# Performance work log

Hardware: AMD Instinct MI355X
Metric: run time of the kernel (lower is better)

## Reference

```python
import jax, jax.numpy as jnp
import numpy as np

B, T, H, W, P = 2, 4, 224, 224, 16
D, DI, NS, RK, KC = 768, 1536, 16, 48, 4
DEPTH = 16
NV, NA = 196, 24                 # video/audio patches per frame
NTOT = (NV + 2 + NA + 2) * T     # 896 tokens (cls + patches + global, both modalities)
LVIS = NTOT // 2                 # 448 visible tokens


def setup_inputs():
    key = jax.random.key(0)
    ks = iter(jax.random.split(key, 64))
    def nrm(shape, s=0.02):
        return jax.random.normal(next(ks), shape, jnp.float32) * s
    inp = {}
    inp['x_v'] = jax.random.normal(next(ks), (B, 3, T, H, W), jnp.float32)
    inp['x_a'] = jax.random.normal(next(ks), (B, 64, 96 * T), jnp.float32)
    inp['patch_v_w'] = nrm((D, 3, P, P)); inp['patch_v_b'] = jnp.zeros((D,), jnp.float32)
    inp['patch_a_w'] = nrm((D, 1, P, P)); inp['patch_a_b'] = jnp.zeros((D,), jnp.float32)
    inp['pos_v'] = nrm((1, NV, D)); inp['pos_a'] = nrm((1, NA, D))
    inp['tpos_v'] = nrm((1, T, D)); inp['tpos_a'] = nrm((1, T, D))
    inp['cls_v'] = nrm((1, 1, D)); inp['cls_a'] = nrm((1, 1, D))
    inp['glob_v'] = nrm((1, 1, D)); inp['glob_a'] = nrm((1, 1, D))
    inp['norm_w'] = jnp.ones((DEPTH, D), jnp.float32)
    inp['in_w'] = nrm((DEPTH, 2 * DI, D))
    inp['conv_w'] = nrm((DEPTH, DI, KC), 0.2); inp['conv_b'] = jnp.zeros((DEPTH, DI), jnp.float32)
    inp['conv_w_b'] = nrm((DEPTH, DI, KC), 0.2); inp['conv_b_b'] = jnp.zeros((DEPTH, DI), jnp.float32)
    inp['xproj_w'] = nrm((DEPTH, RK + 2 * NS, DI))
    inp['xproj_w_b'] = nrm((DEPTH, RK + 2 * NS, DI))
    inp['dt_w'] = nrm((DEPTH, DI, RK), 0.1)
    inp['dt_w_b'] = nrm((DEPTH, DI, RK), 0.1)
    # mamba dt-bias init: inverse-softplus of dt ~ logU[1e-3, 0.1]
    lo, hi = np.log(1e-3), np.log(0.1)
    u = jax.random.uniform(next(ks), (DEPTH, DI), jnp.float32)
    dt = jnp.exp(u * (hi - lo) + lo)
    inp['dt_b'] = dt + jnp.log(-jnp.expm1(-dt))
    u2 = jax.random.uniform(next(ks), (DEPTH, DI), jnp.float32)
    dt2 = jnp.exp(u2 * (hi - lo) + lo)
    inp['dt_b_b'] = dt2 + jnp.log(-jnp.expm1(-dt2))
    alog = jnp.log(jnp.arange(1, NS + 1, dtype=jnp.float32))  # S4D-real init
    inp['A_log'] = jnp.broadcast_to(alog, (DEPTH, DI, NS)) + 0.0
    inp['A_log_b'] = jnp.broadcast_to(alog, (DEPTH, DI, NS)) + 0.0
    inp['D_par'] = jnp.ones((DEPTH, DI), jnp.float32)
    inp['D_par_b'] = jnp.ones((DEPTH, DI), jnp.float32)
    inp['out_w'] = nrm((DEPTH, D, DI))
    rng = np.random.default_rng(0)
    vi = np.stack([np.sort(rng.choice(NTOT, LVIS, replace=False)) for _ in range(B)])
    inp['vis_idx'] = jnp.asarray(vi, jnp.int32)
    return inp


def _causal_conv1d(x, w, b):
    # x: [B,L,DI]; depthwise causal conv, kernel KC
    xt = x.transpose(0, 2, 1)
    y = jax.lax.conv_general_dilated(xt, w[:, None, :], (1,), [(KC - 1, 0)], feature_group_count=DI)
    return (y + b[None, :, None]).transpose(0, 2, 1)


def _ssd(xc, dt, Bm, Cm, A, Dp):
    # selective scan: xc,dt [B,L,DI]; Bm,Cm [B,L,NS]; A [DI,NS]
    dA = jnp.exp(dt[..., None] * A)                         # B,L,DI,NS
    dBx = dt[..., None] * Bm[:, :, None, :] * xc[..., None]
    def step(h, s):
        a, bx, c = s
        h = a * h + bx
        return h, jnp.einsum('bdn,bn->bd', h, c)
    h0 = jnp.zeros((xc.shape[0], DI, NS), xc.dtype)
    _, ys = jax.lax.scan(step, h0, (jnp.swapaxes(dA, 0, 1), jnp.swapaxes(dBx, 0, 1), jnp.swapaxes(Cm, 0, 1)))
    return jnp.swapaxes(ys, 0, 1) + xc * Dp


def _mamba_dir(xi, zi, cw, cb, xw, dw, db, alog, dp):
    xc = jax.nn.silu(_causal_conv1d(xi, cw, cb))
    proj = jnp.einsum('bld,ed->ble', xc, xw)
    dtr, Bm, Cm = jnp.split(proj, [RK, RK + NS], axis=-1)
    dt = jax.nn.softplus(jnp.einsum('blr,dr->bld', dtr, dw) + db)
    y = _ssd(xc, dt, Bm, Cm, -jnp.exp(alog), dp)
    return y * jax.nn.silu(zi)


def reference(x_v, x_a, patch_v_w, patch_v_b, patch_a_w, patch_a_b, pos_v, pos_a, tpos_v, tpos_a,
              cls_v, cls_a, glob_v, glob_a, norm_w, in_w, conv_w, conv_b, conv_w_b, conv_b_b,
              xproj_w, xproj_w_b, dt_w, dt_b, dt_w_b, dt_b_b, A_log, A_log_b, D_par, D_par_b,
              out_w, vis_idx):
    Bn = x_v.shape[0]
    # video patch embed: conv3d k=(1,16,16) as unfold + matmul
    xv = x_v.transpose(0, 2, 3, 4, 1).reshape(Bn, T, H // P, P, W // P, P, 3)
    xv = xv.transpose(0, 1, 2, 4, 3, 5, 6).reshape(Bn, T, NV, P * P * 3)
    wv = patch_v_w.transpose(0, 2, 3, 1).reshape(D, -1)   # (kh,kw,c) flattening order
    xv = xv @ wv.T + patch_v_b                            # B,T,196,D
    # audio patch embed: [B,64,TA] -> [B,1,TA,64] conv2d 16x16
    TA = x_a.shape[-1]
    xa = x_a.transpose(0, 2, 1).reshape(Bn, TA // P, P, 64 // P, P)
    xa = xa.transpose(0, 1, 3, 2, 4).reshape(Bn, (TA // P) * (64 // P), P * P)
    xa = xa @ patch_a_w.reshape(D, -1).T + patch_a_b      # B, T*24, D
    xa = xa.reshape(Bn, T, NA, D)
    # spatial + temporal positional embeddings
    xv = xv + pos_v[None] + tpos_v[:, :, None, :]
    xa = xa + pos_a[None] + tpos_a[:, :, None, :]
    def add_tokens(x, cls, glob):
        BT = x.shape[0]
        return jnp.concatenate([jnp.broadcast_to(cls, (BT, 1, D)), x, jnp.broadcast_to(glob, (BT, 1, D))], 1)
    xv = add_tokens(xv.reshape(Bn * T, NV, D), cls_v, glob_v).reshape(Bn, T, NV + 2, D)
    xa = add_tokens(xa.reshape(Bn * T, NA, D), cls_a, glob_a).reshape(Bn, T, NA + 2, D)
    x = jnp.concatenate([xv, xa], 2).reshape(Bn, -1, D)   # B, 896, D
    x_vis = jnp.take_along_axis(x, vis_idx[:, :, None], axis=1)  # B, 448, D (x[~mask])

    def layer(carry, p):
        h, res = carry
        nw, iw, cw, cb, cwb, cbb, xw, xwb, dw, db, dwb, dbb, al, alb, dp, dpb, ow = p
        res = h + res                                     # fused add (drop_path=identity at eval)
        hn = res * jax.lax.rsqrt(jnp.mean(res * res, -1, keepdims=True) + 1e-5) * nw  # RMSNorm
        xz = jnp.einsum('bld,ed->ble', hn, iw)
        xi, zi = jnp.split(xz, 2, axis=-1)
        yf = _mamba_dir(xi, zi, cw, cb, xw, dw, db, al, dp)
        yb = _mamba_dir(xi[:, ::-1], zi[:, ::-1], cwb, cbb, xwb, dwb, dbb, alb, dpb)
        h = jnp.einsum('bld,ed->ble', yf + yb[:, ::-1], ow)
        return (h, res), None

    carry = (x_vis, jnp.zeros_like(x_vis))
    (h, res), _ = jax.lax.scan(layer, carry, (norm_w, in_w, conv_w, conv_b, conv_w_b, conv_b_b,
                                              xproj_w, xproj_w_b, dt_w, dt_b, dt_w_b, dt_b_b,
                                              A_log, A_log_b, D_par, D_par_b, out_w))
    # clip_return_layer=1 -> return_index=[depth-1]; only the post-loop append of the
    # final residual fires, so forward_features returns stack([residual]) of shape [1,B,L,D]
    return res[None]
```

## Files before the change

### kernel.cpp

```cpp
#include <hip/hip_runtime.h>
#include <math.h>

typedef unsigned short ushort_t;
typedef __attribute__((ext_vector_type(8))) short bf16x8;
typedef __attribute__((ext_vector_type(4))) float f32x4;
typedef __attribute__((ext_vector_type(4))) unsigned short us4;

#define NBATCH 2
#define TT 4
#define DD 768
#define DI_ 1536
#define NS_ 16
#define RK_ 48
#define KC_ 4
#define DEPTH_ 16
#define NRUN 15
#define LV 448
#define NROWS (NBATCH*LV)
#define NCH 7
#define CLEN 64
#define WLAYER 4128768
#define WL4 (WLAYER/4)

__device__ __forceinline__ float silu_f(float x) { return x / (1.f + __expf(-x)); }
__device__ __forceinline__ ushort_t f2bf(float x) {
  unsigned int u = __float_as_uint(x);
  return (ushort_t)((u + 0x7FFFu + ((u >> 16) & 1u)) >> 16);
}
__device__ __forceinline__ float bf2f(ushort_t h) {
  return __uint_as_float(((unsigned int)h) << 16);
}

typedef const __attribute__((address_space(1))) unsigned int* gas1_t;
typedef __attribute__((address_space(3))) unsigned int* las3_t;
__device__ __forceinline__ void gll16(const ushort_t* g, ushort_t* l) {
  __builtin_amdgcn_global_load_lds((gas1_t)g, (las3_t)l, 16, 0, 0);
}

__global__ __launch_bounds__(256) void mfma_gemm(
    const ushort_t* __restrict__ A, const ushort_t* __restrict__ A2, int lda,
    const ushort_t* __restrict__ W, const ushort_t* __restrict__ W2, int ldw,
    const float* __restrict__ bias, const float* __restrict__ bias2,
    float* __restrict__ C, float* __restrict__ C2, int ldc,
    int M, int K, int nkChunks, long partStride, int epi)
{
  int z = blockIdx.z;
  int dir = z / nkChunks, chunk = z - dir * nkChunks;
  if (dir) { A = A2; W = W2; C = C2; bias = bias2; }
  int kChunk = K / nkChunks;
  int kbeg = chunk * kChunk;
  if (nkChunks > 1) C += (long)chunk * partStride;

  __shared__ __align__(16) ushort_t At[128 * 32];
  __shared__ __align__(16) ushort_t Bt[128 * 32];

  int tid = threadIdx.x, wv = tid >> 6, lane = tid & 63;
  int m0 = blockIdx.y * 128, n0 = blockIdx.x * 128;

  int S0 = wv * 128 + lane, S1 = S0 + 64;
  int r0 = S0 >> 2, g0 = (S0 & 3) ^ ((r0 >> 1) & 3);
  int r1 = S1 >> 2, g1 = (S1 & 3) ^ ((r1 >> 1) & 3);
  const ushort_t* a0 = A + (size_t)min(m0 + r0, M - 1) * lda + g0 * 8 + kbeg;
  const ushort_t* a1 = A + (size_t)min(m0 + r1, M - 1) * lda + g1 * 8 + kbeg;
  const ushort_t* b0 = W + (size_t)(n0 + r0) * ldw + g0 * 8 + kbeg;
  const ushort_t* b1 = W + (size_t)(n0 + r1) * ldw + g1 * 8 + kbeg;
  ushort_t* lA0 = At + S0 * 8; ushort_t* lA1 = At + S1 * 8;
  ushort_t* lB0 = Bt + S0 * 8; ushort_t* lB1 = Bt + S1 * 8;

  int wr = wv >> 1, wc = wv & 1;
  int rl = lane & 15, gl = lane >> 4;
  int offA[4], offB[4];
#pragma unroll
  for (int i = 0; i < 4; ++i) {
    int ra = wr * 64 + i * 16 + rl;
    offA[i] = ra * 32 + ((gl ^ ((ra >> 1) & 3)) * 8);
    int rb = wc * 64 + i * 16 + rl;
    offB[i] = rb * 32 + ((gl ^ ((rb >> 1) & 3)) * 8);
  }

  f32x4 acc[4][4] = {};
  int nk = kChunk >> 5;
  for (int t = 0; t < nk; ++t) {
    int ko = t << 5;
    gll16(a0 + ko, lA0); gll16(a1 + ko, lA1);
    gll16(b0 + ko, lB0); gll16(b1 + ko, lB1);
    __syncthreads();
    bf16x8 af[4], bw[4];
#pragma unroll
    for (int i = 0; i < 4; ++i) {
      af[i] = *(const bf16x8*)(At + offA[i]);
      bw[i] = *(const bf16x8*)(Bt + offB[i]);
    }
#pragma unroll
    for (int i = 0; i < 4; ++i)
#pragma unroll
      for (int j = 0; j < 4; ++j)
        acc[i][j] = __builtin_amdgcn_mfma_f32_16x16x32_bf16(af[i], bw[j], acc[i][j], 0, 0, 0);
    __syncthreads();
  }

#pragma unroll
  for (int i = 0; i < 4; ++i) {
    int row0 = m0 + wr * 64 + i * 16 + gl * 4;
#pragma unroll
    for (int q = 0; q < 4; ++q) {
      int row = row0 + q;
      if (row >= M) continue;
#pragma unroll
      for (int j = 0; j < 4; ++j) {
        int col = n0 + wc * 64 + j * 16 + rl;
        float v = acc[i][j][q];
        if (bias) v += bias[col];
        if (epi == 1) v = (v > 20.f) ? v : log1pf(__expf(v));
        if (epi == 2) ((ushort_t*)C)[(size_t)row * ldc + col] = f2bf(v);
        else C[(size_t)row * ldc + col] = v;
      }
    }
  }
}

__global__ __launch_bounds__(256) void gemm_nt(
    const float* __restrict__ A, int lda,
    const float* __restrict__ W, int ldw,
    const float* __restrict__ bias,
    float* __restrict__ C, int ldc, int M, int N, int K)
{
  __shared__ float As[16][68];
  __shared__ float Ws[16][68];
  int tid = threadIdx.x;
  int m0 = blockIdx.y * 64, n0 = blockIdx.x * 64;
  int ty = tid >> 4, tx = tid & 15;
  float acc[4][4] = {};
  for (int k0 = 0; k0 < K; k0 += 16) {
#pragma unroll
    for (int i = 0; i < 4; ++i) {
      int idx = tid + i * 256;
      int mm = idx >> 4, kk = idx & 15;
      int gm = m0 + mm, gk = k0 + kk;
      As[kk][mm] = (gm < M && gk < K) ? A[(size_t)gm * lda + gk] : 0.f;
      int gn = n0 + mm;
      Ws[kk][mm] = (gn < N && gk < K) ? W[(size_t)gn * ldw + gk] : 0.f;
    }
    __syncthreads();
#pragma unroll
    for (int kk = 0; kk < 16; ++kk) {
      float a[4], b[4];
#pragma unroll
      for (int i = 0; i < 4; ++i) a[i] = As[kk][ty * 4 + i];
#pragma unroll
      for (int j = 0; j < 4; ++j) b[j] = Ws[kk][tx * 4 + j];
#pragma unroll
      for (int i = 0; i < 4; ++i)
#pragma unroll
        for (int j = 0; j < 4; ++j) acc[i][j] = fmaf(a[i], b[j], acc[i][j]);
    }
    __syncthreads();
  }
#pragma unroll
  for (int i = 0; i < 4; ++i) {
    int gm = m0 + ty * 4 + i;
    if (gm >= M) continue;
#pragma unroll
    for (int j = 0; j < 4; ++j) {
      int gn = n0 + tx * 4 + j;
      if (gn >= N) continue;
      float v = acc[i][j];
      if (bias) v += bias[gn];
      C[(size_t)gm * ldc + gn] = v;
    }
  }
}

__global__ __launch_bounds__(256) void cast4_k(const float* __restrict__ s, ushort_t* __restrict__ d, int n4)
{
  int i = blockIdx.x * 256 + threadIdx.x;
  if (i >= n4) return;
  f32x4 v = *(const f32x4*)(s + i * 4);
  us4 o = { f2bf(v[0]), f2bf(v[1]), f2bf(v[2]), f2bf(v[3]) };
  *(us4*)(d + i * 4) = o;
}

__global__ __launch_bounds__(256) void cast_all4_k(
    const float* __restrict__ iw0, const float* __restrict__ ow0,
    const float* __restrict__ xw0, const float* __restrict__ xwb0,
    const float* __restrict__ dw0, const float* __restrict__ dwb0,
    ushort_t* __restrict__ wall, int nl)
{
  int i = blockIdx.x * 256 + threadIdx.x;
  if (i >= nl * WL4) return;
  int l = i / WL4;
  int j = (i - l * WL4) * 4;
  const float* iw  = iw0  + (size_t)l * 2359296;
  const float* ow  = ow0  + (size_t)l * 1179648;
  const float* xw  = xw0  + (size_t)l * 122880;
  const float* xwb = xwb0 + (size_t)l * 122880;
  const float* dw  = dw0  + (size_t)l * 73728;
  const float* dwb = dwb0 + (size_t)l * 73728;
  ushort_t* wb = wall + (size_t)l * WLAYER + j;
  f32x4 v = {0.f, 0.f, 0.f, 0.f};
  int j2 = j;
  if (j2 < 2359296) v = *(const f32x4*)(iw + j2);
  else {
    j2 -= 2359296;
    if (j2 < 1179648) v = *(const f32x4*)(ow + j2);
    else {
      j2 -= 1179648;
      if (j2 < 196608) { int r = j2 / 1536, k = j2 - r * 1536;
        if (r < 80) v = *(const f32x4*)(xw + r * 1536 + k); }
      else {
        j2 -= 196608;
        if (j2 < 196608) { int r = j2 / 1536, k = j2 - r * 1536;
          if (r < 80) v = *(const f32x4*)(xwb + r * 1536 + k); }
        else {
          j2 -= 196608;
          if (j2 < 98304) { int d = j2 >> 6, k = j2 & 63;
            if (k < 48) v = *(const f32x4*)(dw + d * 48 + k); }
          else { j2 -= 98304; int d = j2 >> 6, k = j2 & 63;
            if (k < 48) v = *(const f32x4*)(dwb + d * 48 + k); }
        }
      }
    }
  }
  us4 o = { f2bf(v[0]), f2bf(v[1]), f2bf(v[2]), f2bf(v[3]) };
  *(us4*)wb = o;
}

__global__ __launch_bounds__(256) void im2col_v(const float* __restrict__ xv, ushort_t* __restrict__ Av)
{
  int i = blockIdx.x * 256 + threadIdx.x;
  if (i >= 1568 * 768) return;
  int m = i / 768, k = i % 768;
  int c = k >> 8, r = k & 255;
  int kh = r >> 4, kw = r & 15;
  int bt = m / 196, n = m % 196;
  int b = bt / TT, t = bt % TT;
  int hb = n / 14, wb = n % 14;
  Av[i] = f2bf(xv[(size_t)b * 602112 + (size_t)c * 200704 + t * 50176 + (hb * 16 + kh) * 224 + wb * 16 + kw]);
}

__global__ __launch_bounds__(256) void im2col_a(const float* __restrict__ xa, float* __restrict__ Aa)
{
  int i = blockIdx.x * 256 + threadIdx.x;
  if (i >= 192 * 256) return;
  int m = i / 256, k = i % 256;
  int kh = k >> 4, kw = k & 15;
  int b = m / 96, q = m % 96;
  int tb = q >> 2, fb = q & 3;
  Aa[i] = xa[(size_t)b * 24576 + (fb * 16 + kw) * 384 + tb * 16 + kh];
}

__global__ __launch_bounds__(256) void assemble_k(
    const float* __restrict__ tokv, const float* __restrict__ toka,
    const float* __restrict__ pos_v, const float* __restrict__ pos_a,
    const float* __restrict__ tpos_v, const float* __restrict__ tpos_a,
    const float* __restrict__ cls_v, const float* __restrict__ cls_a,
    const float* __restrict__ glob_v, const float* __restrict__ glob_a,
    const int* __restrict__ vis_idx,
    float* __restrict__ h, float* __restrict__ res)
{
  int i = blockIdx.x * 256 + threadIdx.x;
  if (i >= NROWS * DD) return;
  int d = i % DD;
  int bl = i / DD;
  int r = bl % LV, b = bl / LV;
  int tok = vis_idx[b * LV + r];
  int t = tok / 224, q = tok % 224;
  float v;
  if (q == 0) v = cls_v[d];
  else if (q <= 196) {
    int n = q - 1;
    v = tokv[((size_t)(b * TT + t) * 196 + n) * DD + d] + pos_v[n * DD + d] + tpos_v[t * DD + d];
  } else if (q == 197) v = glob_v[d];
  else if (q == 198) v = cls_a[d];
  else if (q <= 222) {
    int n = q - 199;
    v = toka[((size_t)b * 96 + t * 24 + n) * DD + d] + pos_a[n * DD + d] + tpos_a[t * DD + d];
  } else v = glob_a[d];
  h[i] = v;
  res[i] = 0.f;
}

__global__ __launch_bounds__(256) void rmsnorm_k(
    const float* __restrict__ hsrc, const float* __restrict__ part,
    float* __restrict__ res, ushort_t* __restrict__ hn, const float* __restrict__ nw)
{
  int row = blockIdx.x;
  float* rp = res + (size_t)row * DD;
  ushort_t* op = hn + (size_t)row * DD;
  int tid = threadIdx.x;
  float v[3];
  float ss = 0.f;
#pragma unroll
  for (int i = 0; i < 3; ++i) {
    int c = tid + i * 256;
    float x;
    if (part) {
      x = part[(size_t)row * DD + c] + part[688128 + (size_t)row * DD + c]
        + part[2 * 688128 + (size_t)row * DD + c] + part[3 * 688128 + (size_t)row * DD + c];
    } else {
      x = hsrc[(size_t)row * DD + c];
    }
    x += rp[c];
    v[i] = x;
    ss += x * x;
  }
  for (int m = 1; m < 64; m <<= 1) ss += __shfl_xor(ss, m, 64);
  __shared__ float sred[4];
  if ((tid & 63) == 0) sred[tid >> 6] = ss;
  __syncthreads();
  float tot = sred[0] + sred[1] + sred[2] + sred[3];
  float sc = rsqrtf(tot / (float)DD + 1e-5f);
#pragma unroll
  for (int i = 0; i < 3; ++i) {
    int c = tid + i * 256;
    rp[c] = v[i];
    op[c] = f2bf(v[i] * sc * nw[c]);
  }
}

__global__ __launch_bounds__(256) void conv_k(
    const ushort_t* __restrict__ xz,
    const float* __restrict__ cw, const float* __restrict__ cb,
    const float* __restrict__ cwb, const float* __restrict__ cbb,
    ushort_t* __restrict__ xcFb, ushort_t* __restrict__ xcBb)
{
  int i = blockIdx.x * 256 + threadIdx.x;
  if (i >= NROWS * DI_) return;
  int d = i % DI_;
  int bl = i / DI_;
  int l = bl % LV, b = bl / LV;
  const ushort_t* xzb = xz + (size_t)b * LV * (2 * DI_);
  float accf = cb[d];
#pragma unroll
  for (int j = 0; j < 4; ++j) {
    int lp = l - 3 + j;
    if (lp >= 0) accf += bf2f(xzb[(size_t)lp * (2 * DI_) + d]) * cw[d * 4 + j];
  }
  float accb = cbb[d];
#pragma unroll
  for (int j = 0; j < 4; ++j) {
    int lp = l - 3 + j;
    if (lp >= 0) accb += bf2f(xzb[(size_t)(LV - 1 - lp) * (2 * DI_) + d]) * cwb[d * 4 + j];
  }
  xcFb[i] = f2bf(silu_f(accf));
  xcBb[i] = f2bf(silu_f(accb));
}

__global__ __launch_bounds__(256) void reduce_pack_k(
    const float* __restrict__ pF, const float* __restrict__ pB,
    float* __restrict__ prF, float* __restrict__ prB,
    ushort_t* __restrict__ dF, ushort_t* __restrict__ dB)
{
  int i = blockIdx.x * 256 + threadIdx.x;
  if (i >= NROWS * 128) return;
  int dir = blockIdx.y;
  const float* part = dir ? pB : pF;
  float* proj = dir ? prB : prF;
  ushort_t* dtr = dir ? dB : dF;
  int row = i >> 7, col = i & 127;
  float s = 0.f;
  if (col < 80) {
#pragma unroll
    for (int c = 0; c < 8; ++c) s += part[c * (NROWS * 128) + i];
    proj[row * 80 + col] = s;
  }
  if (col < 64) dtr[(row << 6) + col] = f2bf(col < 48 ? s : 0.f);
}

__global__ __launch_bounds__(256) void scanA_k(
    const ushort_t* __restrict__ xcFb, const float* __restrict__ dtF, const float* __restrict__ prF,
    const ushort_t* __restrict__ xcBb, const float* __restrict__ dtB, const float* __restrict__ prB,
    const float* __restrict__ AlF, const float* __restrict__ AlB,
    float* __restrict__ hloc, float* __restrict__ Pb)
{
  int dir = blockIdx.z;
  const ushort_t* xc = dir ? xcBb : xcFb;
  const float* dt = dir ? dtB : dtF;
  const float* pr = dir ? prB : prF;
  const float* Al = dir ? AlB : AlF;
  int c = blockIdx.y;
  int g = blockIdx.x * 16 + (threadIdx.x >> 4);
  int n = threadIdx.x & 15;
  int b = g / DI_, d = g % DI_;
  float An = -__expf(Al[d * NS_ + n]);
  const ushort_t* xcp = xc + (size_t)b * LV * DI_ + d;
  const float* dtp = dt + (size_t)b * LV * DI_ + d;
  const float* prp = pr + (size_t)b * LV * 80;
  int l0 = c * CLEN;
  float hs = 0.f, S = 0.f;
  float dtv = dtp[(size_t)l0 * DI_];
  float xcv = bf2f(xcp[(size_t)l0 * DI_]);
  float bn  = prp[l0 * 80 + 48 + n];
  for (int kk = 0; kk < CLEN; ++kk) {
    float dtv_n = 0.f, xcv_n = 0.f, bn_n = 0.f;
    if (kk < CLEN - 1) {
      int l1 = l0 + kk + 1;
      dtv_n = dtp[(size_t)l1 * DI_];
      xcv_n = bf2f(xcp[(size_t)l1 * DI_]);
      bn_n  = prp[l1 * 80 + 48 + n];
    }
    hs = __expf(dtv * An) * hs + dtv * bn * xcv;
    S += dtv;
    dtv = dtv_n; xcv = xcv_n; bn = bn_n;
  }
  int idx = ((dir * 3072 + g) * 6 + c) * NS_ + n;
  hloc[idx] = hs;
  Pb[idx] = __expf(An * S);
}

__global__ __launch_bounds__(256) void scanBC_k(
    const ushort_t* __restrict__ xcFb, const float* __restrict__ dtF, const float* __restrict__ prF,
    const ushort_t* __restrict__ xcBb, const float* __restrict__ dtB, const float* __restrict__ prB,
    const float* __restrict__ AlF, const float* __restrict__ AlB,
    const float* __restrict__ DpF, const float* __restrict__ DpB,
    const float* __restrict__ hloc, const float* __restrict__ Pb,
    const ushort_t* __restrict__ xz, ushort_t* __restrict__ yc)
{
  int c = blockIdx.y;
  int tid = threadIdx.x;
  int n = tid & 15, gi = (tid >> 4) & 7, dir = tid >> 7;
  int g = blockIdx.x * 8 + gi;
  int b = g / DI_, d = g % DI_;
  __shared__ float sbuf[2][8][64];

  const ushort_t* xc = dir ? xcBb : xcFb;
  const float* dt = dir ? dtB : dtF;
  const float* pr = dir ? prB : prF;
  const float* Al = dir ? AlB : AlF;
  const float* Dpp = dir ? DpB : DpF;
  int myc = dir ? (6 - c) : c;
  float An = -__expf(Al[d * NS_ + n]);
  float Dpd = Dpp[d];
  float hs = 0.f;
  for (int j = 0; j < myc; ++j) {
    int idx = ((dir * 3072 + g) * 6 + j) * NS_ + n;
    hs = Pb[idx] * hs + hloc[idx];
  }
  const ushort_t* xcp = xc + (size_t)b * LV * DI_ + d;
  const float* dtp = dt + (size_t)b * LV * DI_ + d;
  const float* prp = pr + (size_t)b * LV * 80;
  int l0 = myc * CLEN;
  float dtv = dtp[(size_t)l0 * DI_];
  float xcv = bf2f(xcp[(size_t)l0 * DI_]);
  float bn  = prp[l0 * 80 + 48 + n];
  float cn  = prp[l0 * 80 + 64 + n];
  for (int kk = 0; kk < CLEN; ++kk) {
    float dtv_n = 0.f, xcv_n = 0.f, bn_n = 0.f, cn_n = 0.f;
    if (kk < CLEN - 1) {
      int l1 = l0 + kk + 1;
      dtv_n = dtp[(size_t)l1 * DI_];
      xcv_n = bf2f(xcp[(size_t)l1 * DI_]);
      bn_n  = prp[l1 * 80 + 48 + n];
      cn_n  = prp[l1 * 80 + 64 + n];
    }
    hs = __expf(dtv * An) * hs + dtv * bn * xcv;
    float p = hs * cn;
    p += __shfl_xor(p, 1, 16);
    p += __shfl_xor(p, 2, 16);
    p += __shfl_xor(p, 4, 16);
    p += __shfl_xor(p, 8, 16);
    if (n == 0) {
      int off = dir ? (CLEN - 1 - kk) : kk;
      sbuf[dir][gi][off] = p + xcv * Dpd;
    }
    dtv = dtv_n; xcv = xcv_n; bn = bn_n; cn = cn_n;
  }
  __syncthreads();
  for (int oid = tid; oid < 512; oid += 256) {
    int gi2 = oid >> 6, kk = oid & 63;
    int g2 = blockIdx.x * 8 + gi2;
    int b2 = g2 / DI_, d2 = g2 % DI_;
    int l = c * CLEN + kk;
    float z = bf2f(xz[((size_t)b2 * LV + l) * 3072 + 1536 + d2]);
    float v = (sbuf[0][gi2][kk] + sbuf[1][gi2][kk]) * silu_f(z);
    yc[((size_t)b2 * LV + l) * DI_ + d2] = f2bf(v);
  }
}

__global__ __launch_bounds__(256) void final_k(
    const float* __restrict__ res, const float* __restrict__ part, float* __restrict__ out)
{
  int i = blockIdx.x * 256 + threadIdx.x;
  if (i >= NROWS * DD) return;
  out[i] = res[i] + part[i] + part[688128 + i] + part[2 * 688128 + i] + part[3 * 688128 + i];
}

extern "C" void kernel_launch(void* const* d_in, const int* in_sizes, int n_in,
                              void* d_out, int out_size, void* d_ws, size_t ws_size,
                              hipStream_t stream)
{
  const float* x_v = (const float*)d_in[0];
  const float* x_a = (const float*)d_in[1];
  const float* patch_v_w = (const float*)d_in[2];
  const float* patch_v_b = (const float*)d_in[3];
  const float* patch_a_w = (const float*)d_in[4];
  const float* patch_a_b = (const float*)d_in[5];
  const float* pos_v = (const float*)d_in[6];
  const float* pos_a = (const float*)d_in[7];
  const float* tpos_v = (const float*)d_in[8];
  const float* tpos_a = (const float*)d_in[9];
  const float* cls_v = (const float*)d_in[10];
  const float* cls_a = (const float*)d_in[11];
  const float* glob_v = (const float*)d_in[12];
  const float* glob_a = (const float*)d_in[13];
  const float* norm_w = (const float*)d_in[14];
  const float* in_w = (const float*)d_in[15];
  const float* conv_w = (const float*)d_in[16];
  const float* conv_b = (const float*)d_in[17];
  const float* conv_w_b = (const float*)d_in[18];
  const float* conv_b_b = (const float*)d_in[19];
  const float* xproj_w = (const float*)d_in[20];
  const float* xproj_w_b = (const float*)d_in[21];
  const float *dt_w, *dt_bias, *dt_w_b, *dt_bias_b;
  if (in_sizes[23] == DEPTH_ * DI_ * RK_) {
    dt_w = (const float*)d_in[22]; dt_w_b = (const float*)d_in[23];
    dt_bias = (const float*)d_in[24]; dt_bias_b = (const float*)d_in[25];
  } else {
    dt_w = (const float*)d_in[22]; dt_bias = (const float*)d_in[23];
    dt_w_b = (const float*)d_in[24]; dt_bias_b = (const float*)d_in[25];
  }
  const float* A_log = (const float*)d_in[26];
  const float* A_log_b = (const float*)d_in[27];
  const float* D_par = (const float*)d_in[28];
  const float* D_par_b = (const float*)d_in[29];
  const float* out_w = (const float*)d_in[30];
  const int* vis_idx = (const int*)d_in[31];

  float* ws = (float*)d_ws;
  float* res   = ws;
  float* hbuf  = ws + 688128;
  float* R1    = ws + 1376256;
  float* R2f   = ws + 4128768;
  float* R3    = ws + 4816896;
  float* xz    = ws + 7569408;
  float* dtF   = ws + 10321920;
  float* dtB   = ws + 11698176;
  float* projF = ws + 13074432;
  float* projB = ws + 13146112;
  float* wPvf  = ws + 13217792;
  float* WALLf = ws + 13512704;

  float* partF = R1;
  float* partB = R1 + 917504;
  float* hloc  = R1;
  float* Pb    = R1 + 589824;
  float* partO = R1;
  float* tokv  = R1;
  float* toka  = R1 + 1204224;
  float* Aa    = R1 + 1351680;
  ushort_t* Av_bf = (ushort_t*)xz;
  ushort_t* wPv   = (ushort_t*)wPvf;
  ushort_t* hn_bf = (ushort_t*)R2f;
  ushort_t* dtrF  = (ushort_t*)R2f;
  ushort_t* dtrB  = ((ushort_t*)R2f) + 57344;
  ushort_t* ycb   = (ushort_t*)R2f;
  ushort_t* xcFb = (ushort_t*)R3;
  ushort_t* xcBb = ((ushort_t*)R3) + 1376256;
  ushort_t* xzb  = (ushort_t*)xz;

  size_t need_big = ((size_t)13512704 + 30965760) * 4;
  int bigws = ws_size >= need_big;
  ushort_t* WALL = (ushort_t*)WALLf;

  dim3 blk(256);

  if (bigws)
    cast_all4_k<<<(NRUN * WL4 + 255) / 256, blk, 0, stream>>>(
        in_w, out_w, xproj_w, xproj_w_b, dt_w, dt_w_b, WALL, NRUN);

  im2col_v<<<4704, blk, 0, stream>>>(x_v, Av_bf);
  cast4_k<<<576, blk, 0, stream>>>(patch_v_w, wPv, 147456);
  im2col_a<<<192, blk, 0, stream>>>(x_a, Aa);
  mfma_gemm<<<dim3(6, 13, 1), blk, 0, stream>>>(Av_bf, nullptr, 768, wPv, nullptr, 768,
                                                patch_v_b, nullptr, tokv, nullptr, 768,
                                                1568, 768, 1, 0, 0);
  gemm_nt<<<dim3(12, 3, 1), blk, 0, stream>>>(Aa, 256, patch_a_w, 256, patch_a_b,
                                              toka, 768, 192, 768, 256);
  assemble_k<<<2688, blk, 0, stream>>>(tokv, toka, pos_v, pos_a, tpos_v, tpos_a,
                                       cls_v, cls_a, glob_v, glob_a, vis_idx, hbuf, res);

  for (int l = 0; l < NRUN; ++l) {
    const float* nw  = norm_w + l * DD;
    const float* cw  = conv_w + l * DI_ * KC_;
    const float* cb  = conv_b + l * DI_;
    const float* cwb = conv_w_b + l * DI_ * KC_;
    const float* cbb = conv_b_b + l * DI_;
    const float* dbi = dt_bias + l * DI_;
    const float* dbib = dt_bias_b + l * DI_;
    const float* al  = A_log + (size_t)l * DI_ * NS_;
    const float* alb = A_log_b + (size_t)l * DI_ * NS_;
    const float* dp  = D_par + l * DI_;
    const float* dpb = D_par_b + l * DI_;

    ushort_t* wb = bigws ? (WALL + (size_t)l * WLAYER) : WALL;
    if (!bigws)
      cast_all4_k<<<(WL4 + 255) / 256, blk, 0, stream>>>(
          in_w + (size_t)l * 2359296, out_w + (size_t)l * 1179648,
          xproj_w + (size_t)l * 122880, xproj_w_b + (size_t)l * 122880,
          dt_w + (size_t)l * 73728, dt_w_b + (size_t)l * 73728, wb, 1);
    ushort_t* wIn  = wb;
    ushort_t* wOut = wIn + 2359296;
    ushort_t* wXF  = wOut + 1179648;
    ushort_t* wXB  = wXF + 196608;
    ushort_t* wDF  = wXB + 196608;
    ushort_t* wDB  = wDF + 98304;

    rmsnorm_k<<<NROWS, blk, 0, stream>>>(hbuf, l ? partO : nullptr, res, hn_bf, nw);
    mfma_gemm<<<dim3(24, 7, 1), blk, 0, stream>>>(hn_bf, nullptr, 768, wIn, nullptr, 768,
                                                  nullptr, nullptr, (float*)xzb, nullptr, 3072,
                                                  NROWS, 768, 1, 0, 2);
    conv_k<<<5376, blk, 0, stream>>>(xzb, cw, cb, cwb, cbb, xcFb, xcBb);
    mfma_gemm<<<dim3(1, 7, 16), blk, 0, stream>>>(xcFb, xcBb, 1536, wXF, wXB, 1536,
                                                  nullptr, nullptr, partF, partB, 128,
                                                  NROWS, 1536, 8, NROWS * 128, 0);
    reduce_pack_k<<<dim3(448, 2, 1), blk, 0, stream>>>(partF, partB, projF, projB, dtrF, dtrB);
    mfma_gemm<<<dim3(12, 7, 2), blk, 0, stream>>>(dtrF, dtrB, 64, wDF, wDB, 64,
                                                  dbi, dbib, dtF, dtB, 1536,
                                                  NROWS, 64, 1, 0, 1);
    scanA_k<<<dim3(192, 6, 2), blk, 0, stream>>>(xcFb, dtF, projF, xcBb, dtB, projB,
                                                 al, alb, hloc, Pb);
    scanBC_k<<<dim3(384, NCH, 1), blk, 0, stream>>>(xcFb, dtF, projF, xcBb, dtB, projB,
                                                    al, alb, dp, dpb, hloc, Pb, xzb, ycb);
    mfma_gemm<<<dim3(6, 7, 4), blk, 0, stream>>>(ycb, nullptr, 1536, wOut, nullptr, 1536,
                                                 nullptr, nullptr, partO, nullptr, 768,
                                                 NROWS, 1536, 4, NROWS * DD, 0);
  }

  final_k<<<2688, blk, 0, stream>>>(res, partO, (float*)d_out);
}
```

Measured before the change: 3.130 ms.

## Fuse dt projection and softplus into scan kernels, drop dt GEMM and buffers

Removes the separate dt_proj MFMA GEMM and its fp32 dt buffers. Each scan kernel now recomputes dt from the 48-rank projection, with each of the 16 lanes per channel doing 3 FMAs and a shuffle reduction, then applies softplus inline. The audio patch GEMM moves to the bf16 MFMA path, and the weight cast kernel goes to 8-wide stores and no longer casts the dt weights. In exchange, both scanA and scanBC redo the dt computation, adding shuffles and a log1p/exp per step to the serial scan loop, and the audio patch embedding now runs in bf16.

After: 6.043 ms. 93.1% more time.

```diff
diff --git a/kernel.cpp b/kernel.cpp
--- a/kernel.cpp
+++ b/kernel.cpp
@@ -5,6 +5,7 @@
 typedef __attribute__((ext_vector_type(8))) short bf16x8;
 typedef __attribute__((ext_vector_type(4))) float f32x4;
 typedef __attribute__((ext_vector_type(4))) unsigned short us4;
+typedef __attribute__((ext_vector_type(8))) unsigned short us8;
 
 #define NBATCH 2
 #define TT 4
@@ -19,8 +20,8 @@
 #define NROWS (NBATCH*LV)
 #define NCH 7
 #define CLEN 64
-#define WLAYER 4128768
-#define WL4 (WLAYER/4)
+#define WLAYER 3932160
+#define WL8 (WLAYER/8)
 
 __device__ __forceinline__ float silu_f(float x) { return x / (1.f + __expf(-x)); }
 __device__ __forceinline__ ushort_t f2bf(float x) {
@@ -119,58 +120,6 @@
   }
 }
 
-__global__ __launch_bounds__(256) void gemm_nt(
-    const float* __restrict__ A, int lda,
-    const float* __restrict__ W, int ldw,
-    const float* __restrict__ bias,
-    float* __restrict__ C, int ldc, int M, int N, int K)
-{
-  __shared__ float As[16][68];
-  __shared__ float Ws[16][68];
-  int tid = threadIdx.x;
-  int m0 = blockIdx.y * 64, n0 = blockIdx.x * 64;
-  int ty = tid >> 4, tx = tid & 15;
-  float acc[4][4] = {};
-  for (int k0 = 0; k0 < K; k0 += 16) {
-#pragma unroll
-    for (int i = 0; i < 4; ++i) {
-      int idx = tid + i * 256;
-      int mm = idx >> 4, kk = idx & 15;
-      int gm = m0 + mm, gk = k0 + kk;
-      As[kk][mm] = (gm < M && gk < K) ? A[(size_t)gm * lda + gk] : 0.f;
-      int gn = n0 + mm;
-      Ws[kk][mm] = (gn < N && gk < K) ? W[(size_t)gn * ldw + gk] : 0.f;
-    }
-    __syncthreads();
-#pragma unroll
-    for (int kk = 0; kk < 16; ++kk) {
-      float a[4], b[4];
-#pragma unroll
-      for (int i = 0; i < 4; ++i) a[i] = As[kk][ty * 4 + i];
-#pragma unroll
-      for (int j = 0; j < 4; ++j) b[j] = Ws[kk][tx * 4 + j];
-#pragma unroll
-      for (int i = 0; i < 4; ++i)
-#pragma unroll
-        for (int j = 0; j < 4; ++j) acc[i][j] = fmaf(a[i], b[j], acc[i][j]);
-    }
-    __syncthreads();
-  }
-#pragma unroll
-  for (int i = 0; i < 4; ++i) {
-    int gm = m0 + ty * 4 + i;
-    if (gm >= M) continue;
-#pragma unroll
-    for (int j = 0; j < 4; ++j) {
-      int gn = n0 + tx * 4 + j;
-      if (gn >= N) continue;
-      float v = acc[i][j];
-      if (bias) v += bias[gn];
-      C[(size_t)gm * ldc + gn] = v;
-    }
-  }
-}
-
 __global__ __launch_bounds__(256) void cast4_k(const float* __restrict__ s, ushort_t* __restrict__ d, int n4)
 {
   int i = blockIdx.x * 256 + threadIdx.x;
@@ -180,49 +129,34 @@
   *(us4*)(d + i * 4) = o;
 }
 
-__global__ __launch_bounds__(256) void cast_all4_k(
+__global__ __launch_bounds__(256) void cast_all8_k(
     const float* __restrict__ iw0, const float* __restrict__ ow0,
     const float* __restrict__ xw0, const float* __restrict__ xwb0,
-    const float* __restrict__ dw0, const float* __restrict__ dwb0,
     ushort_t* __restrict__ wall, int nl)
 {
   int i = blockIdx.x * 256 + threadIdx.x;
-  if (i >= nl * WL4) return;
-  int l = i / WL4;
-  int j = (i - l * WL4) * 4;
-  const float* iw  = iw0  + (size_t)l * 2359296;
-  const float* ow  = ow0  + (size_t)l * 1179648;
-  const float* xw  = xw0  + (size_t)l * 122880;
-  const float* xwb = xwb0 + (size_t)l * 122880;
-  const float* dw  = dw0  + (size_t)l * 73728;
-  const float* dwb = dwb0 + (size_t)l * 73728;
-  ushort_t* wb = wall + (size_t)l * WLAYER + j;
-  f32x4 v = {0.f, 0.f, 0.f, 0.f};
+  if (i >= nl * WL8) return;
+  int l = i / WL8;
+  int j = (i - l * WL8) * 8;
+  const float* src = nullptr;
   int j2 = j;
-  if (j2 < 2359296) v = *(const f32x4*)(iw + j2);
+  if (j2 < 2359296) src = iw0 + (size_t)l * 2359296 + j2;
   else {
     j2 -= 2359296;
-    if (j2 < 1179648) v = *(const f32x4*)(ow + j2);
+    if (j2 < 1179648) src = ow0 + (size_t)l * 1179648 + j2;
     else {
       j2 -= 1179648;
-      if (j2 < 196608) { int r = j2 / 1536, k = j2 - r * 1536;
-        if (r < 80) v = *(const f32x4*)(xw + r * 1536 + k); }
-      else {
-        j2 -= 196608;
-        if (j2 < 196608) { int r = j2 / 1536, k = j2 - r * 1536;
-          if (r < 80) v = *(const f32x4*)(xwb + r * 1536 + k); }
-        else {
-          j2 -= 196608;
-          if (j2 < 98304) { int d = j2 >> 6, k = j2 & 63;
-            if (k < 48) v = *(const f32x4*)(dw + d * 48 + k); }
-          else { j2 -= 98304; int d = j2 >> 6, k = j2 & 63;
-            if (k < 48) v = *(const f32x4*)(dwb + d * 48 + k); }
-        }
-      }
-    }
-  }
-  us4 o = { f2bf(v[0]), f2bf(v[1]), f2bf(v[2]), f2bf(v[3]) };
-  *(us4*)wb = o;
+      const float* xs = xw0 + (size_t)l * 122880;
+      if (j2 >= 196608) { j2 -= 196608; xs = xwb0 + (size_t)l * 122880; }
+      int r = j2 / 1536, k = j2 - r * 1536;
+      if (r < 80) src = xs + r * 1536 + k;
+    }
+  }
+  f32x4 v0 = {0.f, 0.f, 0.f, 0.f}, v1 = {0.f, 0.f, 0.f, 0.f};
+  if (src) { v0 = *(const f32x4*)src; v1 = *(const f32x4*)(src + 4); }
+  us8 o = { f2bf(v0[0]), f2bf(v0[1]), f2bf(v0[2]), f2bf(v0[3]),
+            f2bf(v1[0]), f2bf(v1[1]), f2bf(v1[2]), f2bf(v1[3]) };
+  *(us8*)(wall + (size_t)l * WLAYER + j) = o;
 }
 
 __global__ __launch_bounds__(256) void im2col_v(const float* __restrict__ xv, ushort_t* __restrict__ Av)
@@ -238,7 +172,7 @@
   Av[i] = f2bf(xv[(size_t)b * 602112 + (size_t)c * 200704 + t * 50176 + (hb * 16 + kh) * 224 + wb * 16 + kw]);
 }
 
-__global__ __launch_bounds__(256) void im2col_a(const float* __restrict__ xa, float* __restrict__ Aa)
+__global__ __launch_bounds__(256) void im2col_a(const float* __restrict__ xa, ushort_t* __restrict__ Aa)
 {
   int i = blockIdx.x * 256 + threadIdx.x;
   if (i >= 192 * 256) return;
@@ -246,7 +180,7 @@
   int kh = k >> 4, kw = k & 15;
   int b = m / 96, q = m % 96;
   int tb = q >> 2, fb = q & 3;
-  Aa[i] = xa[(size_t)b * 24576 + (fb * 16 + kw) * 384 + tb * 16 + kh];
+  Aa[i] = f2bf(xa[(size_t)b * 24576 + (fb * 16 + kw) * 384 + tb * 16 + kh]);
 }
 
 __global__ __launch_bounds__(256) void assemble_k(
@@ -346,62 +280,70 @@
   xcBb[i] = f2bf(silu_f(accb));
 }
 
-__global__ __launch_bounds__(256) void reduce_pack_k(
+__global__ __launch_bounds__(256) void reduce_k(
     const float* __restrict__ pF, const float* __restrict__ pB,
-    float* __restrict__ prF, float* __restrict__ prB,
-    ushort_t* __restrict__ dF, ushort_t* __restrict__ dB)
-{
-  int i = blockIdx.x * 256 + threadIdx.x;
-  if (i >= NROWS * 128) return;
+    float* __restrict__ prF, float* __restrict__ prB)
+{
+  int i = blockIdx.x * 256 + threadIdx.x;
+  if (i >= NROWS * 80) return;
   int dir = blockIdx.y;
   const float* part = dir ? pB : pF;
   float* proj = dir ? prB : prF;
-  ushort_t* dtr = dir ? dB : dF;
-  int row = i >> 7, col = i & 127;
+  int row = i / 80, col = i - row * 80;
   float s = 0.f;
-  if (col < 80) {
-#pragma unroll
-    for (int c = 0; c < 8; ++c) s += part[c * (NROWS * 128) + i];
-    proj[row * 80 + col] = s;
-  }
-  if (col < 64) dtr[(row << 6) + col] = f2bf(col < 48 ? s : 0.f);
+#pragma unroll
+  for (int c = 0; c < 8; ++c) s += part[c * (NROWS * 128) + row * 128 + col];
+  proj[i] = s;
 }
 
 __global__ __launch_bounds__(256) void scanA_k(
-    const ushort_t* __restrict__ xcFb, const float* __restrict__ dtF, const float* __restrict__ prF,
-    const ushort_t* __restrict__ xcBb, const float* __restrict__ dtB, const float* __restrict__ prB,
+    const ushort_t* __restrict__ xcFb, const float* __restrict__ prF,
+    const ushort_t* __restrict__ xcBb, const float* __restrict__ prB,
     const float* __restrict__ AlF, const float* __restrict__ AlB,
+    const float* __restrict__ dwF, const float* __restrict__ dwB,
+    const float* __restrict__ dbF, const float* __restrict__ dbB,
     float* __restrict__ hloc, float* __restrict__ Pb)
 {
   int dir = blockIdx.z;
   const ushort_t* xc = dir ? xcBb : xcFb;
-  const float* dt = dir ? dtB : dtF;
   const float* pr = dir ? prB : prF;
   const float* Al = dir ? AlB : AlF;
+  const float* dw = dir ? dwB : dwF;
+  const float* db = dir ? dbB : dbF;
   int c = blockIdx.y;
   int g = blockIdx.x * 16 + (threadIdx.x >> 4);
   int n = threadIdx.x & 15;
   int b = g / DI_, d = g % DI_;
   float An = -__expf(Al[d * NS_ + n]);
+  float w0 = dw[d * 48 + 3 * n], w1 = dw[d * 48 + 3 * n + 1], w2 = dw[d * 48 + 3 * n + 2];
+  float bias = db[d];
   const ushort_t* xcp = xc + (size_t)b * LV * DI_ + d;
-  const float* dtp = dt + (size_t)b * LV * DI_ + d;
   const float* prp = pr + (size_t)b * LV * 80;
   int l0 = c * CLEN;
   float hs = 0.f, S = 0.f;
-  float dtv = dtp[(size_t)l0 * DI_];
+  float bn  = prp[l0 * 80 + 48 + n];
   float xcv = bf2f(xcp[(size_t)l0 * DI_]);
-  float bn  = prp[l0 * 80 + 48 + n];
+  float s0 = prp[l0 * 80 + 3 * n] * w0 + prp[l0 * 80 + 3 * n + 1] * w1 + prp[l0 * 80 + 3 * n + 2] * w2;
+  s0 += __shfl_xor(s0, 1, 16); s0 += __shfl_xor(s0, 2, 16);
+  s0 += __shfl_xor(s0, 4, 16); s0 += __shfl_xor(s0, 8, 16);
+  s0 += bias;
+  float dt = (s0 > 20.f) ? s0 : log1pf(__expf(s0));
   for (int kk = 0; kk < CLEN; ++kk) {
-    float dtv_n = 0.f, xcv_n = 0.f, bn_n = 0.f;
+    float t0n = 0.f, t1n = 0.f, t2n = 0.f, bn_n = 0.f, xcv_n = 0.f;
     if (kk < CLEN - 1) {
       int l1 = l0 + kk + 1;
-      dtv_n = dtp[(size_t)l1 * DI_];
+      t0n = prp[l1 * 80 + 3 * n]; t1n = prp[l1 * 80 + 3 * n + 1]; t2n = prp[l1 * 80 + 3 * n + 2];
+      bn_n = prp[l1 * 80 + 48 + n];
       xcv_n = bf2f(xcp[(size_t)l1 * DI_]);
-      bn_n  = prp[l1 * 80 + 48 + n];
-    }
-    hs = __expf(dtv * An) * hs + dtv * bn * xcv;
-    S += dtv;
-    dtv = dtv_n; xcv = xcv_n; bn = bn_n;
+    }
+    hs = __expf(dt * An) * hs + dt * bn * xcv;
+    S += dt;
+    float sn = t0n * w0 + t1n * w1 + t2n * w2;
+    sn += __shfl_xor(sn, 1, 16); sn += __shfl_xor(sn, 2, 16);
+    sn += __shfl_xor(sn, 4, 16); sn += __shfl_xor(sn, 8, 16);
+    sn += bias;
+    dt = (sn > 20.f) ? sn : log1pf(__expf(sn));
+    bn = bn_n; xcv = xcv_n;
   }
   int idx = ((dir * 3072 + g) * 6 + c) * NS_ + n;
   hloc[idx] = hs;
@@ -409,9 +351,11 @@
 }
 
 __global__ __launch_bounds__(256) void scanBC_k(
-    const ushort_t* __restrict__ xcFb, const float* __restrict__ dtF, const float* __restrict__ prF,
-    const ushort_t* __restrict__ xcBb, const float* __restrict__ dtB, const float* __restrict__ prB,
+    const ushort_t* __restrict__ xcFb, const float* __restrict__ prF,
+    const ushort_t* __restrict__ xcBb, const float* __restrict__ prB,
     const float* __restrict__ AlF, const float* __restrict__ AlB,
+    const float* __restrict__ dwF, const float* __restrict__ dwB,
+    const float* __restrict__ dbF, const float* __restrict__ dbB,
     const float* __restrict__ DpF, const float* __restrict__ DpB,
     const float* __restrict__ hloc, const float* __restrict__ Pb,
     const ushort_t* __restrict__ xz, ushort_t* __restrict__ yc)
@@ -424,12 +368,15 @@
   __shared__ float sbuf[2][8][64];
 
   const ushort_t* xc = dir ? xcBb : xcFb;
-  const float* dt = dir ? dtB : dtF;
   const float* pr = dir ? prB : prF;
   const float* Al = dir ? AlB : AlF;
+  const float* dw = dir ? dwB : dwF;
+  const float* db = dir ? dbB : dbF;
   const float* Dpp = dir ? DpB : DpF;
   int myc = dir ? (6 - c) : c;
   float An = -__expf(Al[d * NS_ + n]);
+  float w0 = dw[d * 48 + 3 * n], w1 = dw[d * 48 + 3 * n + 1], w2 = dw[d * 48 + 3 * n + 2];
+  float bias = db[d];
   float Dpd = Dpp[d];
   float hs = 0.f;
   for (int j = 0; j < myc; ++j) {
@@ -437,23 +384,26 @@
     hs = Pb[idx] * hs + hloc[idx];
   }
   const ushort_t* xcp = xc + (size_t)b * LV * DI_ + d;
-  const float* dtp = dt + (size_t)b * LV * DI_ + d;
   const float* prp = pr + (size_t)b * LV * 80;
   int l0 = myc * CLEN;
-  float dtv = dtp[(size_t)l0 * DI_];
-  float xcv = bf2f(xcp[(size_t)l0 * DI_]);
   float bn  = prp[l0 * 80 + 48 + n];
   float cn  = prp[l0 * 80 + 64 + n];
+  float xcv = bf2f(xcp[(size_t)l0 * DI_]);
+  float s0 = prp[l0 * 80 + 3 * n] * w0 + prp[l0 * 80 + 3 * n + 1] * w1 + prp[l0 * 80 + 3 * n + 2] * w2;
+  s0 += __shfl_xor(s0, 1, 16); s0 += __shfl_xor(s0, 2, 16);
+  s0 += __shfl_xor(s0, 4, 16); s0 += __shfl_xor(s0, 8, 16);
+  s0 += bias;
+  float dt = (s0 > 20.f) ? s0 : log1pf(__expf(s0));
   for (int kk = 0; kk < CLEN; ++kk) {
-    float dtv_n = 0.f, xcv_n = 0.f, bn_n = 0.f, cn_n = 0.f;
+    float t0n = 0.f, t1n = 0.f, t2n = 0.f, bn_n = 0.f, cn_n = 0.f, xcv_n = 0.f;
     if (kk < CLEN - 1) {
       int l1 = l0 + kk + 1;
-      dtv_n = dtp[(size_t)l1 * DI_];
+      t0n = prp[l1 * 80 + 3 * n]; t1n = prp[l1 * 80 + 3 * n + 1]; t2n = prp[l1 * 80 + 3 * n + 2];
+      bn_n = prp[l1 * 80 + 48 + n];
+      cn_n = prp[l1 * 80 + 64 + n];
       xcv_n = bf2f(xcp[(size_t)l1 * DI_]);
-      bn_n  = prp[l1 * 80 + 48 + n];
-      cn_n  = prp[l1 * 80 + 64 + n];
-    }
-    hs = __expf(dtv * An) * hs + dtv * bn * xcv;
+    }
+    hs = __expf(dt * An) * hs + dt * bn * xcv;
     float p = hs * cn;
     p += __shfl_xor(p, 1, 16);
     p += __shfl_xor(p, 2, 16);
@@ -463,7 +413,12 @@
       int off = dir ? (CLEN - 1 - kk) : kk;
       sbuf[dir][gi][off] = p + xcv * Dpd;
     }
-    dtv = dtv_n; xcv = xcv_n; bn = bn_n; cn = cn_n;
+    float sn = t0n * w0 + t1n * w1 + t2n * w2;
+    sn += __shfl_xor(sn, 1, 16); sn += __shfl_xor(sn, 2, 16);
+    sn += __shfl_xor(sn, 4, 16); sn += __shfl_xor(sn, 8, 16);
+    sn += bias;
+    dt = (sn > 20.f) ? sn : log1pf(__expf(sn));
+    bn = bn_n; cn = cn_n; xcv = xcv_n;
   }
   __syncthreads();
   for (int oid = tid; oid < 512; oid += 256) {
@@ -533,8 +488,7 @@
   float* R2f   = ws + 4128768;
   float* R3    = ws + 4816896;
   float* xz    = ws + 7569408;
-  float* dtF   = ws + 10321920;
-  float* dtB   = ws + 11698176;
+  float* scr   = ws + 10321920;
   float* projF = ws + 13074432;
   float* projB = ws + 13146112;
   float* wPvf  = ws + 13217792;
@@ -547,35 +501,36 @@
   float* partO = R1;
   float* tokv  = R1;
   float* toka  = R1 + 1204224;
-  float* Aa    = R1 + 1351680;
   ushort_t* Av_bf = (ushort_t*)xz;
   ushort_t* wPv   = (ushort_t*)wPvf;
+  ushort_t* wPa   = (ushort_t*)scr;
+  ushort_t* Aa_bf = ((ushort_t*)scr) + 196608;
   ushort_t* hn_bf = (ushort_t*)R2f;
-  ushort_t* dtrF  = (ushort_t*)R2f;
-  ushort_t* dtrB  = ((ushort_t*)R2f) + 57344;
   ushort_t* ycb   = (ushort_t*)R2f;
   ushort_t* xcFb = (ushort_t*)R3;
   ushort_t* xcBb = ((ushort_t*)R3) + 1376256;
   ushort_t* xzb  = (ushort_t*)xz;
 
-  size_t need_big = ((size_t)13512704 + 30965760) * 4;
+  size_t need_big = ((size_t)13512704 + (size_t)NRUN * (WLAYER / 2)) * 4;
   int bigws = ws_size >= need_big;
   ushort_t* WALL = (ushort_t*)WALLf;
 
   dim3 blk(256);
 
   if (bigws)
-    cast_all4_k<<<(NRUN * WL4 + 255) / 256, blk, 0, stream>>>(
-        in_w, out_w, xproj_w, xproj_w_b, dt_w, dt_w_b, WALL, NRUN);
+    cast_all8_k<<<(NRUN * WL8 + 255) / 256, blk, 0, stream>>>(
+        in_w, out_w, xproj_w, xproj_w_b, WALL, NRUN);
 
   im2col_v<<<4704, blk, 0, stream>>>(x_v, Av_bf);
   cast4_k<<<576, blk, 0, stream>>>(patch_v_w, wPv, 147456);
-  im2col_a<<<192, blk, 0, stream>>>(x_a, Aa);
+  cast4_k<<<192, blk, 0, stream>>>(patch_a_w, wPa, 49152);
+  im2col_a<<<192, blk, 0, stream>>>(x_a, Aa_bf);
   mfma_gemm<<<dim3(6, 13, 1), blk, 0, stream>>>(Av_bf, nullptr, 768, wPv, nullptr, 768,
                                                 patch_v_b, nullptr, tokv, nullptr, 768,
                                                 1568, 768, 1, 0, 0);
-  gemm_nt<<<dim3(12, 3, 1), blk, 0, stream>>>(Aa, 256, patch_a_w, 256, patch_a_b,
-                                              toka, 768, 192, 768, 256);
+  mfma_gemm<<<dim3(6, 2, 1), blk, 0, stream>>>(Aa_bf, nullptr, 256, wPa, nullptr, 256,
+                                               patch_a_b, nullptr, toka, nullptr, 768,
+                                               192, 256, 1, 0, 0);
   assemble_k<<<2688, blk, 0, stream>>>(tokv, toka, pos_v, pos_a, tpos_v, tpos_a,
                                        cls_v, cls_a, glob_v, glob_a, vis_idx, hbuf, res);
 
@@ -585,6 +540,8 @@
     const float* cb  = conv_b + l * DI_;
     const float* cwb = conv_w_b + l * DI_ * KC_;
     const float* cbb = conv_b_b + l * DI_;
+    const float* dwF = dt_w + (size_t)l * DI_ * RK_;
+    const float* dwB = dt_w_b + (size_t)l * DI_ * RK_;
     const float* dbi = dt_bias + l * DI_;
     const float* dbib = dt_bias_b + l * DI_;
     const float* al  = A_log + (size_t)l * DI_ * NS_;
@@ -594,16 +551,13 @@
 
     ushort_t* wb = bigws ? (WALL + (size_t)l * WLAYER) : WALL;
     if (!bigws)
-      cast_all4_k<<<(WL4 + 255) / 256, blk, 0, stream>>>(
+      cast_all8_k<<<(WL8 + 255) / 256, blk, 0, stream>>>(
           in_w + (size_t)l * 2359296, out_w + (size_t)l * 1179648,
-          xproj_w + (size_t)l * 122880, xproj_w_b + (size_t)l * 122880,
-          dt_w + (size_t)l * 73728, dt_w_b + (size_t)l * 73728, wb, 1);
+          xproj_w + (size_t)l * 122880, xproj_w_b + (size_t)l * 122880, wb, 1);
     ushort_t* wIn  = wb;
     ushort_t* wOut = wIn + 2359296;
     ushort_t* wXF  = wOut + 1179648;
     ushort_t* wXB  = wXF + 196608;
-    ushort_t* wDF  = wXB + 196608;
-    ushort_t* wDB  = wDF + 98304;
 
     rmsnorm_k<<<NROWS, blk, 0, stream>>>(hbuf, l ? partO : nullptr, res, hn_bf, nw);
     mfma_gemm<<<dim3(24, 7, 1), blk, 0, stream>>>(hn_bf, nullptr, 768, wIn, nullptr, 768,
@@ -613,14 +567,12 @@
     mfma_gemm<<<dim3(1, 7, 16), blk, 0, stream>>>(xcFb, xcBb, 1536, wXF, wXB, 1536,
                                                   nullptr, nullptr, partF, partB, 128,
                                                   NROWS, 1536, 8, NROWS * 128, 0);
-    reduce_pack_k<<<dim3(448, 2, 1), blk, 0, stream>>>(partF, partB, projF, projB, dtrF, dtrB);
-    mfma_gemm<<<dim3(12, 7, 2), blk, 0, stream>>>(dtrF, dtrB, 64, wDF, wDB, 64,
-                                                  dbi, dbib, dtF, dtB, 1536,
-                                                  NROWS, 64, 1, 0, 1);
-    scanA_k<<<dim3(192, 6, 2), blk, 0, stream>>>(xcFb, dtF, projF, xcBb, dtB, projB,
-                                                 al, alb, hloc, Pb);
-    scanBC_k<<<dim3(384, NCH, 1), blk, 0, stream>>>(xcFb, dtF, projF, xcBb, dtB, projB,
-                                                    al, alb, dp, dpb, hloc, Pb, xzb, ycb);
+    reduce_k<<<dim3(280, 2, 1), blk, 0, stream>>>(partF, partB, projF, projB);
+    scanA_k<<<dim3(192, 6, 2), blk, 0, stream>>>(xcFb, projF, xcBb, projB,
+                                                 al, alb, dwF, dwB, dbi, dbib, hloc, Pb);
+    scanBC_k<<<dim3(384, NCH, 1), blk, 0, stream>>>(xcFb, projF, xcBb, projB,
+                                                    al, alb, dwF, dwB, dbi, dbib,
+                                                    dp, dpb, hloc, Pb, xzb, ycb);
     mfma_gemm<<<dim3(6, 7, 4), blk, 0, stream>>>(ycb, nullptr, 1536, wOut, nullptr, 1536,
                                                  nullptr, nullptr, partO, nullptr, 768,
                                                  NROWS, 1536, 4, NROWS * DD, 0);
```
